# Kernel optimization log

Measured on AMD Instinct MI355X. Metric: run time of the kernel, lower is better.

The kernel has to match this reference:

```python
import jax, jax.numpy as jnp
import numpy as np

B, S, D_IN, D_MODEL = 128, 2048, 512, 2048
M, NSY, H, T = 25, 64, 8, 10
REP = NSY * (NSY + 1) // 2
OUT_DIMS = S * 2
DH = D_IN // H
IU, JU = np.triu_indices(NSY)
IDX_OUT = np.arange(NSY)                      # 'first-last': first n neurons for out sync
IDX_ACT = np.arange(D_MODEL - NSY, D_MODEL)   # last n neurons for action sync


def _ln(x, g, b):
    mu = x.mean(-1, keepdims=True)
    var = x.var(-1, keepdims=True)
    return (x - mu) / jnp.sqrt(var + 1e-5) * g + b


def _sync(act, alpha, beta, r, idx):
    # pairwise upper-triangle outer product without materializing (B,n,n)
    sel = act[:, idx]
    pair = sel[:, IU] * sel[:, JU]  # (B, REP)
    if alpha is None:
        alpha, beta = pair, jnp.ones_like(pair)
    else:
        alpha = r * alpha + pair
        beta = r * beta + 1.0
    return alpha / jnp.sqrt(beta), alpha, beta


def _forward(tokens, emb, W_pos, b_pos, Wq, bq, Wk, bk, Wv, bv, Wo, bo, Ws, bs,
             ln_s_g, ln_s_b, ln_n_g, ln_n_b, Wn, bn, temp, Wout, bout,
             start_act, start_trace, decay_action, decay_out):
    # rotary-style learned positional embedding: rotate [0,1] by theta in [0,180deg]
    thetas = jnp.deg2rad(jnp.linspace(0.0, 180.0, S))
    rotated = jnp.stack([-jnp.sin(thetas), jnp.cos(thetas)], -1)  # (S,2)
    pe = rotated @ W_pos + b_pos                                   # (S, D_IN)
    feats = emb[tokens] + pe[None]                                 # (B,S,D_IN)
    kh = (feats @ Wk + bk).reshape(B, S, H, DH)
    vh = (feats @ Wv + bv).reshape(B, S, H, DH)
    r_a = jnp.exp(-decay_action)[None]
    r_o = jnp.exp(-decay_out)[None]
    act = jnp.broadcast_to(start_act[None], (B, D_MODEL))
    trace = jnp.broadcast_to(start_trace[None], (B, D_MODEL, M))
    a_a = b_a = a_o = b_o = None
    preds, certs = [], []
    for _ in range(T):
        s_act, a_a, b_a = _sync(act, a_a, b_a, r_a, IDX_ACT)
        q = (s_act @ Wq + bq).reshape(B, H, DH)
        scores = jnp.einsum('bhd,bshd->bhs', q, kh) / np.float32(np.sqrt(DH))
        attn = jax.nn.softmax(scores, -1)
        o = jnp.einsum('bhs,bshd->bhd', attn, vh).reshape(B, D_IN) @ Wo + bo
        # SynapseNet: Linear -> GLU -> LayerNorm
        pre = jnp.concatenate([o, act], -1) @ Ws + bs
        g1, g2 = jnp.split(pre, 2, -1)
        state = _ln(g1 * jax.nn.sigmoid(g2), ln_s_g, ln_s_b)  # (B, D_MODEL)
        trace = jnp.concatenate([trace[:, :, 1:], state[:, :, None]], -1)
        # NLM: per-neuron linear over memory, GLU, temperature
        xn = _ln(trace, ln_n_g, ln_n_b)
        y = jnp.einsum('bnm,mon->bno', xn, Wn) + bn  # (B, D_MODEL, 2)
        act = (y[..., 0] * jax.nn.sigmoid(y[..., 1])) / temp
        s_out, a_o, b_o = _sync(act, a_o, b_o, r_o, IDX_OUT)
        pred = s_out @ Wout + bout  # (B, OUT_DIMS)
        preds.append(pred)
        logits = pred.reshape(B, S, 2)
        p = jax.nn.softmax(logits, -1)
        ent = -(p * jax.nn.log_softmax(logits, -1)).sum(-1) / np.float32(np.log(2.0))
        ne = ent.mean(-1)
        certs.append(jnp.stack([ne, 1.0 - ne], -1))
    return jnp.stack(preds, -1), jnp.stack(certs, -1)  # (B,OUT_DIMS,T),(B,2,T)


def setup_inputs() -> dict:
    key = jax.random.key(0)
    ks = jax.random.split(key, 16)
    def n(k, shape, s=0.02):
        return (jax.random.normal(k, shape) * s).astype(jnp.float32)
    bound = 1.0 / np.sqrt(M + 2)
    return {
        'tokens': jax.random.randint(ks[0], (B, S), 0, 2, dtype=jnp.int32),
        'emb': n(ks[1], (2, D_IN), 1.0),
        'W_pos': n(ks[2], (2, D_IN)), 'b_pos': jnp.zeros((D_IN,)),
        'Wq': n(ks[3], (REP, D_IN)), 'bq': jnp.zeros((D_IN,)),
        'Wk': n(ks[4], (D_IN, D_IN)), 'bk': jnp.zeros((D_IN,)),
        'Wv': n(ks[5], (D_IN, D_IN)), 'bv': jnp.zeros((D_IN,)),
        'Wo': n(ks[6], (D_IN, D_IN)), 'bo': jnp.zeros((D_IN,)),
        'Ws': n(ks[7], (D_IN + D_MODEL, 2 * D_MODEL)), 'bs': jnp.zeros((2 * D_MODEL,)),
        'ln_s_g': jnp.ones((D_MODEL,)), 'ln_s_b': jnp.zeros((D_MODEL,)),
        'ln_n_g': jnp.ones((M,)), 'ln_n_b': jnp.zeros((M,)),
        'Wn': jax.random.uniform(ks[8], (M, 2, D_MODEL), minval=-bound, maxval=bound),
        'bn': jnp.zeros((1, D_MODEL, 2)),
        'temp': jnp.ones((1,)),
        'Wout': n(ks[9], (REP, OUT_DIMS)), 'bout': jnp.zeros((OUT_DIMS,)),
        'start_act': n(ks[10], (D_MODEL,), 1.0),
        'start_trace': n(ks[11], (D_MODEL, M), 1.0),
        'decay_action': jax.random.uniform(ks[12], (REP,), minval=0.0, maxval=1.0),
        'decay_out': jax.random.uniform(ks[13], (REP,), minval=0.0, maxval=1.0),
    }


def reference(tokens, emb, W_pos, b_pos, Wq, bq, Wk, bk, Wv, bv, Wo, bo, Ws, bs,
              ln_s_g, ln_s_b, ln_n_g, ln_n_b, Wn, bn, temp, Wout, bout,
              start_act, start_trace, decay_action, decay_out):
    return _forward(tokens, emb, W_pos, b_pos, Wq, bq, Wk, bk, Wv, bv, Wo, bo, Ws, bs,
                    ln_s_g, ln_s_b, ln_n_g, ln_n_b, Wn, bn, temp, Wout, bout,
                    start_act, start_trace, decay_action, decay_out)
```

## Files before the change

kernel.cpp:

```cpp
#include <hip/hip_runtime.h>
#include <hip/hip_bf16.h>
#include <math.h>

#define B_ 128
#define S_ 2048
#define D_IN_ 512
#define D_MODEL_ 2048
#define M_ 25
#define NSY_ 64
#define H_ 8
#define T_ 10
#define REP_ 2080
#define DH_ 64
#define PRED_N (B_ * 4096)

typedef unsigned short ushort_t;
typedef __bf16 bf16x8 __attribute__((ext_vector_type(8)));
typedef float f32x4 __attribute__((ext_vector_type(4)));
typedef unsigned short us8 __attribute__((ext_vector_type(8)));
typedef unsigned short us4 __attribute__((ext_vector_type(4)));

__device__ __forceinline__ ushort_t f2bf(float f) {
    __hip_bfloat16 h = __float2bfloat16(f);
    return *(ushort_t*)&h;
}

__global__ __launch_bounds__(256) void gemm_bf16(
    const float* __restrict__ A, int lda,
    const ushort_t* __restrict__ Bt, int ldb,
    const float* __restrict__ bias,
    float* __restrict__ C, int ldc,
    int M, int N, int K, int kchunk)
{
    const int nb = blockIdx.x, mb = blockIdx.y, zb = blockIdx.z;
    const int k0 = zb * kchunk;
    const int k1 = min(K, k0 + kchunk);
    __shared__ ushort_t As[64][40];
    __shared__ ushort_t Bs[128][40];

    const int tid  = threadIdx.x;
    const int wave = tid >> 6;
    const int lane = tid & 63;
    const int quad = lane >> 4;
    const int mrow = lane & 15;

    f32x4 acc[4][2];
    #pragma unroll
    for (int s = 0; s < 4; s++)
        #pragma unroll
        for (int u = 0; u < 2; u++)
            acc[s][u] = (f32x4){0.f, 0.f, 0.f, 0.f};

    const int arow = tid >> 2, akc = (tid & 3) * 8;
    const int brow = tid >> 1, bkc = (tid & 1) * 16;

    for (int kk0 = k0; kk0 < k1; kk0 += 32) {
        {
            const float* ap = A + (size_t)(mb * 64 + arow) * lda + kk0 + akc;
            float4 v0 = *(const float4*)ap;
            float4 v1 = *(const float4*)(ap + 4);
            us8 w = { f2bf(v0.x), f2bf(v0.y), f2bf(v0.z), f2bf(v0.w),
                      f2bf(v1.x), f2bf(v1.y), f2bf(v1.z), f2bf(v1.w) };
            *(us8*)&As[arow][akc] = w;
        }
        {
            const ushort_t* bp = Bt + (size_t)(nb * 128 + brow) * ldb + kk0 + bkc;
            *(us8*)&Bs[brow][bkc]     = *(const us8*)bp;
            *(us8*)&Bs[brow][bkc + 8] = *(const us8*)(bp + 8);
        }
        __syncthreads();

        bf16x8 af[4], bfr[2];
        #pragma unroll
        for (int s = 0; s < 4; s++)
            af[s] = *(const bf16x8*)&As[s * 16 + mrow][quad * 8];
        #pragma unroll
        for (int u = 0; u < 2; u++)
            bfr[u] = *(const bf16x8*)&Bs[wave * 32 + u * 16 + mrow][quad * 8];
        #pragma unroll
        for (int s = 0; s < 4; s++)
            #pragma unroll
            for (int u = 0; u < 2; u++)
                acc[s][u] = __builtin_amdgcn_mfma_f32_16x16x32_bf16(
                    af[s], bfr[u], acc[s][u], 0, 0, 0);
        __syncthreads();
    }

    if (gridDim.z == 1) {
        #pragma unroll
        for (int s = 0; s < 4; s++)
            #pragma unroll
            for (int u = 0; u < 2; u++) {
                const int col = nb * 128 + wave * 32 + u * 16 + mrow;
                #pragma unroll
                for (int reg = 0; reg < 4; reg++) {
                    const int row = mb * 64 + s * 16 + quad * 4 + reg;
                    C[(size_t)row * ldc + col] = acc[s][u][reg] + bias[col];
                }
            }
    } else {
        #pragma unroll
        for (int s = 0; s < 4; s++)
            #pragma unroll
            for (int u = 0; u < 2; u++) {
                const int col = nb * 128 + wave * 32 + u * 16 + mrow;
                #pragma unroll
                for (int reg = 0; reg < 4; reg++) {
                    const int row = mb * 64 + s * 16 + quad * 4 + reg;
                    atomicAdd(&C[(size_t)row * ldc + col], acc[s][u][reg]);
                }
            }
    }
}

__global__ __launch_bounds__(256) void gemm3_kernel(
    const float* __restrict__ f2,
    const ushort_t* __restrict__ WkT, const float* __restrict__ bk, float* __restrict__ Ktab,
    const ushort_t* __restrict__ WvT, const float* __restrict__ bv, float* __restrict__ Vtab,
    const ushort_t* __restrict__ WsT, const ushort_t* __restrict__ WoC,
    const float* __restrict__ zerov, float* __restrict__ Wcomb32)
{
    const int nb = blockIdx.x, mb = blockIdx.y, zs = blockIdx.z;
    const ushort_t* Bt = (zs == 0) ? WkT : (zs == 1) ? WvT : WoC;
    const float* bias  = (zs == 0) ? bk  : (zs == 1) ? bv  : zerov;
    float* C           = (zs == 0) ? Ktab : (zs == 1) ? Vtab : Wcomb32;

    __shared__ ushort_t As[64][40];
    __shared__ ushort_t Bs[128][40];

    const int tid  = threadIdx.x;
    const int wave = tid >> 6;
    const int lane = tid & 63;
    const int quad = lane >> 4;
    const int mrow = lane & 15;

    f32x4 acc[4][2];
    #pragma unroll
    for (int s = 0; s < 4; s++)
        #pragma unroll
        for (int u = 0; u < 2; u++)
            acc[s][u] = (f32x4){0.f, 0.f, 0.f, 0.f};

    const int arow = tid >> 2, akc = (tid & 3) * 8;
    const int brow = tid >> 1, bkc = (tid & 1) * 16;

    for (int kk0 = 0; kk0 < 512; kk0 += 32) {
        if (zs < 2) {
            const float* ap = f2 + (size_t)(mb * 64 + arow) * 512 + kk0 + akc;
            float4 v0 = *(const float4*)ap;
            float4 v1 = *(const float4*)(ap + 4);
            us8 w = { f2bf(v0.x), f2bf(v0.y), f2bf(v0.z), f2bf(v0.w),
                      f2bf(v1.x), f2bf(v1.y), f2bf(v1.z), f2bf(v1.w) };
            *(us8*)&As[arow][akc] = w;
        } else {
            const ushort_t* ap = WsT + (size_t)(mb * 64 + arow) * 2560 + kk0 + akc;
            *(us8*)&As[arow][akc] = *(const us8*)ap;
        }
        {
            const ushort_t* bp = Bt + (size_t)(nb * 128 + brow) * 512 + kk0 + bkc;
            *(us8*)&Bs[brow][bkc]     = *(const us8*)bp;
            *(us8*)&Bs[brow][bkc + 8] = *(const us8*)(bp + 8);
        }
        __syncthreads();

        bf16x8 af[4], bfr[2];
        #pragma unroll
        for (int s = 0; s < 4; s++)
            af[s] = *(const bf16x8*)&As[s * 16 + mrow][quad * 8];
        #pragma unroll
        for (int u = 0; u < 2; u++)
            bfr[u] = *(const bf16x8*)&Bs[wave * 32 + u * 16 + mrow][quad * 8];
        #pragma unroll
        for (int s = 0; s < 4; s++)
            #pragma unroll
            for (int u = 0; u < 2; u++)
                acc[s][u] = __builtin_amdgcn_mfma_f32_16x16x32_bf16(
                    af[s], bfr[u], acc[s][u], 0, 0, 0);
        __syncthreads();
    }

    #pragma unroll
    for (int s = 0; s < 4; s++)
        #pragma unroll
        for (int u = 0; u < 2; u++) {
            const int col = nb * 128 + wave * 32 + u * 16 + mrow;
            #pragma unroll
            for (int reg = 0; reg < 4; reg++) {
                const int row = mb * 64 + s * 16 + quad * 4 + reg;
                C[(size_t)row * 512 + col] = acc[s][u][reg] + bias[col];
            }
        }
}

__device__ __forceinline__ void g_tile128(
    const ushort_t* Ap, int lda, const ushort_t* Bt, int ldb,
    float* C, int ldc, int nb, int mb, int k0, int k1, char* smem, int tid)
{
    ushort_t (*As)[40] = (ushort_t(*)[40])smem;
    ushort_t (*Bs)[40] = (ushort_t(*)[40])(smem + 64 * 40 * 2);
    const int wave = tid >> 6;
    const int lane = tid & 63;
    const int quad = lane >> 4;
    const int mrow = lane & 15;

    f32x4 acc[4][2];
    #pragma unroll
    for (int s = 0; s < 4; s++)
        #pragma unroll
        for (int u = 0; u < 2; u++)
            acc[s][u] = (f32x4){0.f, 0.f, 0.f, 0.f};

    const int arow = tid >> 2, akc = (tid & 3) * 8;
    const int brow = tid >> 1, bkc = (tid & 1) * 16;

    for (int kk0 = k0; kk0 < k1; kk0 += 32) {
        {
            const ushort_t* ap = Ap + (size_t)(mb * 64 + arow) * lda + kk0 + akc;
            *(us8*)&As[arow][akc] = *(const us8*)ap;
        }
        {
            const ushort_t* bp = Bt + (size_t)(nb * 128 + brow) * ldb + kk0 + bkc;
            *(us8*)&Bs[brow][bkc]     = *(const us8*)bp;
            *(us8*)&Bs[brow][bkc + 8] = *(const us8*)(bp + 8);
        }
        __syncthreads();

        bf16x8 af[4], bfr[2];
        #pragma unroll
        for (int s = 0; s < 4; s++)
            af[s] = *(const bf16x8*)&As[s * 16 + mrow][quad * 8];
        #pragma unroll
        for (int u = 0; u < 2; u++)
            bfr[u] = *(const bf16x8*)&Bs[wave * 32 + u * 16 + mrow][quad * 8];
        #pragma unroll
        for (int s = 0; s < 4; s++)
            #pragma unroll
            for (int u = 0; u < 2; u++)
                acc[s][u] = __builtin_amdgcn_mfma_f32_16x16x32_bf16(
                    af[s], bfr[u], acc[s][u], 0, 0, 0);
        __syncthreads();
    }

    #pragma unroll
    for (int s = 0; s < 4; s++)
        #pragma unroll
        for (int u = 0; u < 2; u++) {
            const int col = nb * 128 + wave * 32 + u * 16 + mrow;
            #pragma unroll
            for (int reg = 0; reg < 4; reg++) {
                const int row = mb * 64 + s * 16 + quad * 4 + reg;
                atomicAdd(&C[(size_t)row * ldc + col], acc[s][u][reg]);
            }
        }
}

__global__ __launch_bounds__(256) void triple_kernel(
    const ushort_t* __restrict__ s_outb, const ushort_t* __restrict__ WoutT,
    float* __restrict__ predt,
    const ushort_t* __restrict__ s_actb, const ushort_t* __restrict__ WqT,
    float* __restrict__ qbuf,
    const ushort_t* __restrict__ actb, const ushort_t* __restrict__ WsT,
    float* __restrict__ pre_nxt)
{
    __shared__ __align__(16) char smem[15360];
    const int vb = blockIdx.x, tid = threadIdx.x;
    if (vb < 320) {
        const int nb = vb & 31, mb = (vb >> 5) & 1, zb = vb >> 6;
        const int k0 = zb * 416;
        g_tile128(s_outb, REP_, WoutT, REP_, predt, 4096,
                  nb, mb, k0, min(REP_, k0 + 416), smem, tid);
    } else if (vb < 424) {
        const int v2 = vb - 320;
        const int nb = v2 & 3, mb = (v2 >> 2) & 1, zb = v2 >> 3;
        const int k0 = zb * 160;
        g_tile128(s_actb, REP_, WqT, REP_, qbuf, 512,
                  nb, mb, k0, min(REP_, k0 + 160), smem, tid);
    } else {
        const int v3 = vb - 424;
        const int nb = v3 & 31, mb = (v3 >> 5) & 1, zb = v3 >> 6;
        const int k0 = zb * 256;
        g_tile128(actb, 2048, WsT + 512, 2560, pre_nxt, 4096,
                  nb, mb, k0, k0 + 256, smem, tid);
    }
}

__global__ __launch_bounds__(256) void dual0_kernel(
    const ushort_t* __restrict__ actb, const ushort_t* __restrict__ WsT,
    float* __restrict__ pre0,
    const ushort_t* __restrict__ s_actb, const ushort_t* __restrict__ WqT,
    float* __restrict__ qbuf)
{
    __shared__ __align__(16) char smem[15360];
    const int vb = blockIdx.x, tid = threadIdx.x;
    if (vb < 512) {
        const int nb = vb & 31, mb = (vb >> 5) & 1, zb = vb >> 6;
        const int k0 = zb * 256;
        g_tile128(actb, 2048, WsT + 512, 2560, pre0, 4096,
                  nb, mb, k0, k0 + 256, smem, tid);
    } else {
        const int v2 = vb - 512;
        const int nb = v2 & 3, mb = (v2 >> 2) & 1, zb = v2 >> 3;
        const int k0 = zb * 160;
        g_tile128(s_actb, REP_, WqT, REP_, qbuf, 512,
                  nb, mb, k0, min(REP_, k0 + 160), smem, tid);
    }
}

__global__ __launch_bounds__(256) void gemm_qk_sel(
    const float* __restrict__ q,
    const ushort_t* __restrict__ Kb,
    const unsigned* __restrict__ tokbit,
    float* __restrict__ scsel)
{
    const int nb = blockIdx.x, mb = blockIdx.y, z = blockIdx.z;
    const int c = z >> 3, h = z & 7;
    __shared__ ushort_t As[64][40];
    __shared__ ushort_t Bs[128][40];

    const int tid  = threadIdx.x;
    const int wave = tid >> 6;
    const int lane = tid & 63;
    const int quad = lane >> 4;
    const int mrow = lane & 15;

    f32x4 acc[4][2];
    #pragma unroll
    for (int s = 0; s < 4; s++)
        #pragma unroll
        for (int u = 0; u < 2; u++)
            acc[s][u] = (f32x4){0.f, 0.f, 0.f, 0.f};

    const int arow = tid >> 2, akc = (tid & 3) * 8;
    const int brow = tid >> 1, bkc = (tid & 1) * 16;
    const float* Abase = q + (size_t)h * 64;
    const ushort_t* Bbase = Kb + (size_t)c * S_ * 512 + h * 64;

    #pragma unroll
    for (int kk0 = 0; kk0 < 64; kk0 += 32) {
        {
            const float* ap = Abase + (size_t)(mb * 64 + arow) * 512 + kk0 + akc;
            float4 v0 = *(const float4*)ap;
            float4 v1 = *(const float4*)(ap + 4);
            us8 w = { f2bf(v0.x), f2bf(v0.y), f2bf(v0.z), f2bf(v0.w),
                      f2bf(v1.x), f2bf(v1.y), f2bf(v1.z), f2bf(v1.w) };
            *(us8*)&As[arow][akc] = w;
        }
        {
            const ushort_t* bp = Bbase + (size_t)(nb * 128 + brow) * 512 + kk0 + bkc;
            *(us8*)&Bs[brow][bkc]     = *(const us8*)bp;
            *(us8*)&Bs[brow][bkc + 8] = *(const us8*)(bp + 8);
        }
        __syncthreads();

        bf16x8 af[4], bfr[2];
        #pragma unroll
        for (int s = 0; s < 4; s++)
            af[s] = *(const bf16x8*)&As[s * 16 + mrow][quad * 8];
        #pragma unroll
        for (int u = 0; u < 2; u++)
            bfr[u] = *(const bf16x8*)&Bs[wave * 32 + u * 16 + mrow][quad * 8];
        #pragma unroll
        for (int s = 0; s < 4; s++)
            #pragma unroll
            for (int u = 0; u < 2; u++)
                acc[s][u] = __builtin_amdgcn_mfma_f32_16x16x32_bf16(
                    af[s], bfr[u], acc[s][u], 0, 0, 0);
        __syncthreads();
    }

    const int colw = nb * 4 + wave;
    unsigned tb[16];
    #pragma unroll
    for (int s = 0; s < 4; s++)
        #pragma unroll
        for (int reg = 0; reg < 4; reg++) {
            const int row = mb * 64 + s * 16 + quad * 4 + reg;
            tb[s * 4 + reg] = tokbit[row * 64 + colw];
        }

    float* Cb = scsel + (size_t)h * 128 * S_;
    #pragma unroll
    for (int s = 0; s < 4; s++)
        #pragma unroll
        for (int u = 0; u < 2; u++) {
            const int col = nb * 128 + wave * 32 + u * 16 + mrow;
            const int sh = (u * 16 + mrow) & 31;
            #pragma unroll
            for (int reg = 0; reg < 4; reg++) {
                const int row = mb * 64 + s * 16 + quad * 4 + reg;
                if (((tb[s * 4 + reg] >> sh) & 1u) == (unsigned)c)
                    Cb[(size_t)row * S_ + col] = 0.125f * acc[s][u][reg];
            }
        }
}

__global__ __launch_bounds__(256) void attn_soft(
    const float* __restrict__ scsel,
    const int*   __restrict__ tokens,
    ushort_t* __restrict__ P,
    float* __restrict__ o,
    const float* __restrict__ bs2,
    float* __restrict__ pre_nxt)
{
    const int bh = blockIdx.x;
    const int b = bh >> 3, h = bh & 7;
    __shared__ float red[256];
    const int tid = threadIdx.x;

    if (bh < 512) {
        const int idx = bh * 256 + tid;
        const float4* bs4 = (const float4*)bs2;
        ((float4*)pre_nxt)[idx] = bs4[idx & 1023];
    } else if (bh < 576) {
        const int idx = (bh - 512) * 256 + tid;
        ((float4*)o)[idx] = make_float4(0.f, 0.f, 0.f, 0.f);
    }

    const float* scs = scsel + ((size_t)h * 128 + b) * S_;
    const int* trow = tokens + (size_t)b * S_;

    int tok[8]; float sel[8];
    float lmax = -1e30f;
    #pragma unroll
    for (int i = 0; i < 8; i++) {
        const int s = tid + i * 256;
        tok[i] = trow[s];
        sel[i] = scs[s];
        lmax = fmaxf(lmax, sel[i]);
    }
    red[tid] = lmax; __syncthreads();
    for (int off = 128; off > 0; off >>= 1) {
        if (tid < off) red[tid] = fmaxf(red[tid], red[tid + off]);
        __syncthreads();
    }
    const float mx = red[0];
    __syncthreads();

    float e[8];
    float lsum = 0.f;
    #pragma unroll
    for (int i = 0; i < 8; i++) {
        e[i] = expf(sel[i] - mx);
        lsum += e[i];
    }
    red[tid] = lsum; __syncthreads();
    for (int off = 128; off > 0; off >>= 1) {
        if (tid < off) red[tid] += red[tid + off];
        __syncthreads();
    }
    const float inv = 1.f / red[0];

    ushort_t* Pb = P + ((size_t)h * 128 + b) * 4096;
    #pragma unroll
    for (int i = 0; i < 8; i++) {
        const int s = tid + i * 256;
        const unsigned p = (unsigned)f2bf(e[i] * inv);
        const unsigned word = tok[i] ? (p << 16) : p;
        *(unsigned*)&Pb[s * 2] = word;
    }
}

__global__ __launch_bounds__(256) void gemm_pv(
    const ushort_t* __restrict__ P,
    const ushort_t* __restrict__ VT,
    float* __restrict__ o)
{
    const int mb = blockIdx.x, h = blockIdx.y, zb = blockIdx.z;
    const int k0 = zb * 256;
    __shared__ ushort_t As[64][40];
    __shared__ ushort_t Bs[64][40];

    const int tid  = threadIdx.x;
    const int wave = tid >> 6;
    const int lane = tid & 63;
    const int quad = lane >> 4;
    const int mrow = lane & 15;

    f32x4 acc[4];
    #pragma unroll
    for (int s = 0; s < 4; s++) acc[s] = (f32x4){0.f, 0.f, 0.f, 0.f};

    const int row = tid >> 2, kc = (tid & 3) * 8;
    const ushort_t* Ab = P  + ((size_t)h * 128 + mb * 64 + row) * 4096;
    const ushort_t* Bb = VT + ((size_t)h * 64 + row) * 4096;

    for (int kk = k0; kk < k0 + 256; kk += 32) {
        *(us8*)&As[row][kc] = *(const us8*)(Ab + kk + kc);
        *(us8*)&Bs[row][kc] = *(const us8*)(Bb + kk + kc);
        __syncthreads();
        bf16x8 bfr = *(const bf16x8*)&Bs[wave * 16 + mrow][quad * 8];
        #pragma unroll
        for (int s = 0; s < 4; s++) {
            bf16x8 af = *(const bf16x8*)&As[s * 16 + mrow][quad * 8];
            acc[s] = __builtin_amdgcn_mfma_f32_16x16x32_bf16(af, bfr, acc[s], 0, 0, 0);
        }
        __syncthreads();
    }

    const int col = h * 64 + wave * 16 + mrow;
    #pragma unroll
    for (int s = 0; s < 4; s++)
        #pragma unroll
        for (int reg = 0; reg < 4; reg++) {
            const int rowi = mb * 64 + s * 16 + quad * 4 + reg;
            atomicAdd(&o[(size_t)rowi * 512 + col], acc[s][reg]);
        }
}

#define IA_FE 8192
#define IA_AC (IA_FE + 1024)
#define IA_TR (IA_AC + 6400)
#define IA_SY (IA_TR + 9)
#define IA_ZV (IA_SY + 1)
#define IA_WO (IA_ZV + 256)
#define IA_BS (IA_WO + 16)
#define IA_NB (IA_BS + 1024)
__global__ void init_all(const float* __restrict__ emb, const float* __restrict__ Wp,
                         const float* __restrict__ bp, float* __restrict__ f2,
                         const float* __restrict__ sa, float* __restrict__ act,
                         ushort_t* __restrict__ actb,
                         const float* __restrict__ st, float* __restrict__ trace,
                         const float* __restrict__ dec_act, const float* __restrict__ dec_out,
                         int* __restrict__ ijtab, float* __restrict__ r_act,
                         float* __restrict__ r_out, float* __restrict__ sqb_a,
                         float* __restrict__ sqb_o, float* __restrict__ zerov,
                         const float* __restrict__ Wo, ushort_t* __restrict__ WoC,
                         const float* __restrict__ bs, const float* __restrict__ bo,
                         const float* __restrict__ Ws, float* __restrict__ bs2,
                         const int* __restrict__ tokens, unsigned* __restrict__ tokbit)
{
    const int vb = blockIdx.x, tid = threadIdx.x;
    if (vb < IA_FE) {
        const int gid = vb * 256 + tid;
        const int k = gid & 511;
        const int s = (gid >> 9) & (S_ - 1);
        const int c = gid >> 20;
        const float th = 3.14159265358979323846f * (float)s / (float)(S_ - 1);
        f2[gid] = emb[c * 512 + k] + (-sinf(th)) * Wp[k] + cosf(th) * Wp[512 + k] + bp[k];
    } else if (vb < IA_AC) {
        const int gid = (vb - IA_FE) * 256 + tid;
        const int n = gid & 2047;
        const float v = sa[n];
        act[gid] = v;
        actb[gid] = f2bf(v);
    } else if (vb < IA_TR) {
        const int idx4 = (vb - IA_AC) * 256 + tid;
        ((float4*)trace)[idx4] = ((const float4*)st)[idx4 % 12800];
    } else if (vb < IA_SY) {
        const int p = (vb - IA_TR) * 256 + tid;
        if (p >= REP_) return;
        int i = 0, rem = p;
        while (rem >= NSY_ - i) { rem -= NSY_ - i; i++; }
        ijtab[p] = (i << 16) | (i + rem);
        const float ra = expf(-dec_act[p]);
        const float ro = expf(-dec_out[p]);
        r_act[p] = ra; r_out[p] = ro;
        float ba = 1.f, bo2 = 1.f;
        sqb_a[p] = 1.f;
        sqb_o[p] = 1.f;
        for (int t = 1; t < T_; t++) {
            ba  = ra * ba  + 1.f;
            bo2 = ro * bo2 + 1.f;
            sqb_a[(size_t)t * REP_ + p] = sqrtf(ba);
            sqb_o[(size_t)t * REP_ + p] = sqrtf(bo2);
        }
    } else if (vb < IA_ZV) {
        #pragma unroll
        for (int k = 0; k < 4; k++)
            ((float4*)zerov)[tid * 4 + k] = make_float4(0.f, 0.f, 0.f, 0.f);
    } else if (vb < IA_WO) {
        const int idx4 = (vb - IA_ZV) * 256 + tid;
        float4 v = ((const float4*)Wo)[idx4];
        us4 w = { f2bf(v.x), f2bf(v.y), f2bf(v.z), f2bf(v.w) };
        ((us4*)WoC)[idx4] = w;
    } else if (vb < IA_BS) {
        const int n = (vb - IA_WO) * 256 + tid;
        float acc = bs[n];
        for (int j = 0; j < 512; j++)
            acc += bo[j] * Ws[(size_t)j * 4096 + n];
        bs2[n] = acc;
    } else {
        const int blk = vb - IA_BS;
        const int b = blk >> 3, s0 = (blk & 7) * 256;
        const int tok = tokens[(size_t)b * S_ + s0 + tid];
        const unsigned long long m = __ballot(tok != 0);
        if ((tid & 63) == 0) {
            const int w = tid >> 6;
            tokbit[b * 64 + (s0 >> 5) + w * 2]     = (unsigned)m;
            tokbit[b * 64 + (s0 >> 5) + w * 2 + 1] = (unsigned)(m >> 32);
        }
    }
}

__global__ __launch_bounds__(256) void transpose_all(
    const float* __restrict__ Wk, ushort_t* __restrict__ WkT,
    const float* __restrict__ Wv, ushort_t* __restrict__ WvT,
    const float* __restrict__ Wq, ushort_t* __restrict__ WqT,
    const float* __restrict__ Wo, ushort_t* __restrict__ WoT,
    const float* __restrict__ Ws, ushort_t* __restrict__ WsT,
    const float* __restrict__ Wout, ushort_t* __restrict__ WoutT)
{
    int bid = blockIdx.x;
    const float* in; ushort_t* out; int K, N;
    if      (bid <   256) {              in = Wk;   out = WkT;   K = 512;  N = 512;  }
    else if (bid <   512) { bid -=  256; in = Wv;   out = WvT;   K = 512;  N = 512;  }
    else if (bid <  1552) { bid -=  512; in = Wq;   out = WqT;   K = 2080; N = 512;  }
    else if (bid <  1808) { bid -= 1552; in = Wo;   out = WoT;   K = 512;  N = 512;  }
    else if (bid < 12048) { bid -= 1808; in = Ws;   out = WsT;   K = 2560; N = 4096; }
    else                  { bid -= 12048; in = Wout; out = WoutT; K = 2080; N = 4096; }
    const int bxw = N >> 5;
    const int bx = bid % bxw, by = bid / bxw;
    __shared__ float tile[32][33];
    const int k0 = by * 32, n0 = bx * 32;
    const int tx = threadIdx.x & 31, ty4 = (threadIdx.x >> 5) * 4;
    #pragma unroll
    for (int i = 0; i < 4; i++)
        tile[ty4 + i][tx] = in[(size_t)(k0 + ty4 + i) * N + n0 + tx];
    __syncthreads();
    #pragma unroll
    for (int i = 0; i < 4; i++)
        out[(size_t)(n0 + ty4 + i) * K + k0 + tx] = f2bf(tile[tx][ty4 + i]);
}

__global__ void cast3_kernel(const float* __restrict__ Ktab, ushort_t* __restrict__ Kb,
                             const float* __restrict__ Vtab, ushort_t* __restrict__ VT,
                             const float* __restrict__ Wcomb32, ushort_t* __restrict__ WcombTb)
{
    const int vb = blockIdx.x, tid = threadIdx.x;
    if (vb < 2048) {
        const int idx4 = vb * 256 + tid;
        float4 v = ((const float4*)Ktab)[idx4];
        us4 w = { f2bf(v.x), f2bf(v.y), f2bf(v.z), f2bf(v.w) };
        ((us4*)Kb)[idx4] = w;
    } else if (vb < 10240) {
        const int gid = (vb - 2048) * 256 + tid;
        const int k = gid & 4095;
        const int d = (gid >> 12) & 63;
        const int h = gid >> 18;
        const int s = k >> 1, c = k & 1;
        VT[gid] = f2bf(Vtab[((size_t)(c * S_ + s)) * 512 + h * 64 + d]);
    } else {
        const int idx4 = (vb - 10240) * 256 + tid;
        float4 v = ((const float4*)Wcomb32)[idx4];
        us4 w = { f2bf(v.x), f2bf(v.y), f2bf(v.z), f2bf(v.w) };
        ((us4*)WcombTb)[idx4] = w;
    }
}

__global__ void sync_kernel(const float* __restrict__ act,
                            float* __restrict__ alpha,
                            const float* __restrict__ decay,
                            const int t, const int off,
                            ushort_t* __restrict__ sout,
                            float* __restrict__ ib1, const float* __restrict__ bias1, int iN1,
                            float* __restrict__ ib2, const float* __restrict__ bias2, int iN2)
{
    const int b = blockIdx.x;
    const int tid = threadIdx.x;
    if (blockIdx.y == 8) {
        if (ib1)
            for (int n = tid; n < iN1; n += 256)
                ib1[(size_t)b * iN1 + n] = bias1[n];
        if (ib2)
            for (int n = tid; n < iN2; n += 256)
                ib2[(size_t)b * iN2 + n] = bias2[n];
    }
    const int p = blockIdx.y * 256 + tid;
    if (p >= REP_) return;
    int i = 0, rem = p;
    while (rem >= NSY_ - i) { rem -= NSY_ - i; i++; }
    const int j = i + rem;
    const float si = act[(size_t)b * D_MODEL_ + off + i];
    const float sj = act[(size_t)b * D_MODEL_ + off + j];
    const float pair = si * sj;
    const float r = expf(-decay[p]);
    float a;
    if (t == 0) a = pair;
    else        a = r * alpha[(size_t)b * REP_ + p] + pair;
    alpha[(size_t)b * REP_ + p] = a;
    float bta = 1.f;
    for (int k = 0; k < t; k++) bta = r * bta + 1.f;
    sout[(size_t)b * REP_ + p] = f2bf(a / sqrtf(bta));
}

template<int TT>
__global__ __launch_bounds__(512, 2) void st_kernel(
    const float* __restrict__ pre,
    const float* __restrict__ g,
    const float* __restrict__ bt,
    float* __restrict__ trace,
    const float* __restrict__ ln_g,
    const float* __restrict__ ln_b,
    const float* __restrict__ Wn,
    const float* __restrict__ bn,
    const float* __restrict__ temp,
    ushort_t* __restrict__ actb,
    const int* __restrict__ ijtab,
    const float* __restrict__ r_out,
    const float* __restrict__ sqb_out,
    float* __restrict__ a_o,
    ushort_t* __restrict__ s_outb,
    const float* __restrict__ bout,
    float* __restrict__ predt,
    const float* __restrict__ r_act,
    const float* __restrict__ sqb_act,
    float* __restrict__ a_a,
    ushort_t* __restrict__ s_actb,
    const float* __restrict__ bq,
    float* __restrict__ qbuf)
{
    const int b = blockIdx.x >> 1, half = blockIdx.x & 1;
    const int tid = threadIdx.x;
    __shared__ float v[D_MODEL_];
    __shared__ float r1[512], r2[512];
    __shared__ float sh_sync[64];
    float s1 = 0.f, s2 = 0.f;
    #pragma unroll
    for (int i = 0; i < 4; i++) {
        const int dd = tid + i * 512;
        const float g1 = pre[(size_t)b * 4096 + dd];
        const float g2 = pre[(size_t)b * 4096 + 2048 + dd];
        const float val = g1 * (1.f / (1.f + expf(-g2)));
        v[dd] = val; s1 += val; s2 += val * val;
    }
    r1[tid] = s1; r2[tid] = s2; __syncthreads();
    for (int off = 256; off > 0; off >>= 1) {
        if (tid < off) { r1[tid] += r1[tid + off]; r2[tid] += r2[tid + off]; }
        __syncthreads();
    }
    const float mu = r1[0] * (1.f / D_MODEL_);
    const float var = fmaxf(r2[0] * (1.f / D_MODEL_) - mu * mu, 0.f);
    const float sinv = 1.f / sqrtf(var + 1e-5f);
    const float tval = temp[0];

    #pragma unroll
    for (int i = 0; i < 2; i++) {
        const int n = half * 1024 + i * 512 + tid;
        const float sval = (v[n] - mu) * sinv * g[n] + bt[n];
        const int gid = b * 2048 + n;
        float* tr = trace + (size_t)gid * M_;
        float x[M_];
        #pragma unroll
        for (int m = 0; m < M_ - 1; m++) {
            int slot = TT + 1 + m;
            if (slot >= M_) slot -= M_;
            x[m] = tr[slot];
        }
        x[M_ - 1] = sval;
        tr[TT] = sval;
        float t1 = 0.f, t2 = 0.f;
        #pragma unroll
        for (int m = 0; m < M_; m++) { t1 += x[m]; t2 += x[m] * x[m]; }
        const float tmu = t1 * (1.f / M_);
        const float tvar = fmaxf(t2 * (1.f / M_) - tmu * tmu, 0.f);
        const float tinv = 1.f / sqrtf(tvar + 1e-5f);
        float y0 = bn[n * 2 + 0], y1 = bn[n * 2 + 1];
        #pragma unroll
        for (int m = 0; m < M_; m++) {
            const float xn = (x[m] - tmu) * tinv * ln_g[m] + ln_b[m];
            y0 += xn * Wn[(size_t)(m * 2 + 0) * D_MODEL_ + n];
            y1 += xn * Wn[(size_t)(m * 2 + 1) * D_MODEL_ + n];
        }
        const float a = y0 * (1.f / (1.f + expf(-y1))) / tval;
        actb[gid] = f2bf(a);
        if (half == 0) {
            if (i == 0 && tid < 64) sh_sync[tid] = a;
        } else {
            if (i == 1 && tid >= 448) sh_sync[tid - 448] = a;
        }
    }
    __syncthreads();

    if (half == 0) {
        for (int p = tid; p < REP_; p += 512) {
            const int ij = ijtab[p];
            const float pair = sh_sync[ij >> 16] * sh_sync[ij & 0xffff];
            const float r = r_out[p];
            float a2;
            if (TT == 0) a2 = pair;
            else         a2 = r * a_o[(size_t)b * REP_ + p] + pair;
            a_o[(size_t)b * REP_ + p] = a2;
            s_outb[(size_t)b * REP_ + p] = f2bf(a2 / sqb_out[(size_t)TT * REP_ + p]);
        }
        const float4* b4 = (const float4*)bout;
        float4* pd = (float4*)(predt + (size_t)b * 4096);
        for (int idx = tid; idx < 1024; idx += 512) pd[idx] = b4[idx];
    } else if (TT < T_ - 1) {
        for (int p = tid; p < REP_; p += 512) {
            const int ij = ijtab[p];
            const float pair = sh_sync[ij >> 16] * sh_sync[ij & 0xffff];
            const float r = r_act[p];
            float a2 = r * a_a[(size_t)b * REP_ + p] + pair;
            a_a[(size_t)b * REP_ + p] = a2;
            s_actb[(size_t)b * REP_ + p] = f2bf(a2 / sqb_act[(size_t)(TT + 1) * REP_ + p]);
        }
        const float4* b4 = (const float4*)bq;
        float4* qb = (float4*)(qbuf + (size_t)b * 512);
        if (tid < 128) qb[tid] = b4[tid];
    }
}

__global__ __launch_bounds__(256) void epilogue_kernel(
    const float* __restrict__ predst,
    float* __restrict__ dout)
{
    __shared__ float tile[T_][1024];
    __shared__ float red[256];
    __shared__ float certv[T_];
    const int b = blockIdx.x, tid = threadIdx.x;

    float esum[T_];
    #pragma unroll
    for (int t = 0; t < T_; t++) esum[t] = 0.f;

    for (int c4 = 0; c4 < 4; c4++) {
        const int row0 = c4 * 1024;
        #pragma unroll
        for (int t = 0; t < T_; t++) {
            float4 v = *(const float4*)(predst + (size_t)t * PRED_N
                                        + (size_t)b * 4096 + row0 + tid * 4);
            tile[t][tid * 4 + 0] = v.x; tile[t][tid * 4 + 1] = v.y;
            tile[t][tid * 4 + 2] = v.z; tile[t][tid * 4 + 3] = v.w;
            {
                const float mm = fmaxf(v.x, v.y);
                const float z0 = expf(v.x - mm), z1 = expf(v.y - mm);
                const float Z = z0 + z1, lz = logf(Z);
                const float p0 = z0 / Z, p1 = z1 / Z;
                esum[t] += -(p0 * ((v.x - mm) - lz) + p1 * ((v.y - mm) - lz))
                           * 1.4426950408889634f;
            }
            {
                const float mm = fmaxf(v.z, v.w);
                const float z0 = expf(v.z - mm), z1 = expf(v.w - mm);
                const float Z = z0 + z1, lz = logf(Z);
                const float p0 = z0 / Z, p1 = z1 / Z;
                esum[t] += -(p0 * ((v.z - mm) - lz) + p1 * ((v.w - mm) - lz))
                           * 1.4426950408889634f;
            }
        }
        __syncthreads();
        float buf[40];
        #pragma unroll
        for (int r = 0; r < 4; r++)
            #pragma unroll
            for (int t = 0; t < T_; t++)
                buf[r * 10 + t] = tile[t][tid * 4 + r];
        float* dst = dout + ((size_t)b * 4096 + row0 + tid * 4) * T_;
        #pragma unroll
        for (int k = 0; k < 10; k++)
            *(float4*)(dst + k * 4) = make_float4(buf[4*k], buf[4*k+1], buf[4*k+2], buf[4*k+3]);
        __syncthreads();
    }

    #pragma unroll
    for (int t = 0; t < T_; t++) {
        red[tid] = esum[t]; __syncthreads();
        for (int off = 128; off > 0; off >>= 1) {
            if (tid < off) red[tid] += red[tid + off];
            __syncthreads();
        }
        if (tid == 0) certv[t] = red[0] * (1.f / S_);
        __syncthreads();
    }

    const size_t base = (size_t)PRED_N * T_;
    if (tid < T_)
        dout[base + (size_t)(b * 2 + 0) * T_ + tid] = certv[tid];
    else if (tid < 2 * T_)
        dout[base + (size_t)(b * 2 + 1) * T_ + (tid - T_)] = 1.f - certv[tid - T_];
}

extern "C" void kernel_launch(void* const* d_in, const int* in_sizes, int n_in,
                              void* d_out, int out_size, void* d_ws, size_t ws_size,
                              hipStream_t stream)
{
    const int*   tokens    = (const int*)  d_in[0];
    const float* emb       = (const float*)d_in[1];
    const float* W_pos     = (const float*)d_in[2];
    const float* b_pos     = (const float*)d_in[3];
    const float* Wq        = (const float*)d_in[4];
    const float* bq        = (const float*)d_in[5];
    const float* Wk        = (const float*)d_in[6];
    const float* bk        = (const float*)d_in[7];
    const float* Wv        = (const float*)d_in[8];
    const float* bv        = (const float*)d_in[9];
    const float* Wo        = (const float*)d_in[10];
    const float* bo        = (const float*)d_in[11];
    const float* Ws        = (const float*)d_in[12];
    const float* bs        = (const float*)d_in[13];
    const float* ln_s_g    = (const float*)d_in[14];
    const float* ln_s_b    = (const float*)d_in[15];
    const float* ln_n_g    = (const float*)d_in[16];
    const float* ln_n_b    = (const float*)d_in[17];
    const float* Wn        = (const float*)d_in[18];
    const float* bn        = (const float*)d_in[19];
    const float* temp      = (const float*)d_in[20];
    const float* Wout      = (const float*)d_in[21];
    const float* bout      = (const float*)d_in[22];
    const float* start_act = (const float*)d_in[23];
    const float* start_tr  = (const float*)d_in[24];
    const float* dec_act   = (const float*)d_in[25];
    const float* dec_out   = (const float*)d_in[26];
    float* out = (float*)d_out;
    float* w = (float*)d_ws;

    size_t off = 0;
    float* f2     = w + off; off += (size_t)2 * S_ * 512;
    float* Ktab   = w + off; off += (size_t)2 * S_ * 512;
    float* Vtab   = w + off; off += (size_t)2 * S_ * 512;
    float* act    = w + off; off += (size_t)B_ * D_MODEL_;
    float* a_a    = w + off; off += (size_t)B_ * REP_;
    float* a_o    = w + off; off += (size_t)B_ * REP_;
    float* qbuf   = w + off; off += (size_t)B_ * 512;
    float* o_attn = w + off; off += (size_t)B_ * 512;
    float* pre0   = w + off; off += (size_t)B_ * 4096;
    float* pre1   = w + off; off += (size_t)B_ * 4096;
    float* trace  = w + off; off += (size_t)B_ * D_MODEL_ * M_;
    float* scsel  = w + off; off += (size_t)8 * 128 * S_;
    float* predst = w + off; off += (size_t)T_ * PRED_N;
    float* Wcomb32= w + off; off += (size_t)4096 * 512;
    float* bs2    = w + off; off += 4096;
    float* zerov  = w + off; off += 4096;
    ushort_t* s_actb = (ushort_t*)(w + off); off += (size_t)B_ * REP_ / 2;
    ushort_t* s_outb = (ushort_t*)(w + off); off += (size_t)B_ * REP_ / 2;
    ushort_t* actb   = (ushort_t*)(w + off); off += (size_t)B_ * D_MODEL_ / 2;
    __hip_bfloat16* Kb = (__hip_bfloat16*)(w + off); off += (size_t)S_ * 512;
    ushort_t* Pbuf  = (ushort_t*)(w + off); off += (size_t)8 * 128 * 4096 / 2;
    ushort_t* VT    = (ushort_t*)(w + off); off += (size_t)8 * 64 * 4096 / 2;
    ushort_t* WkT   = (ushort_t*)(w + off); off += (size_t)512 * 512 / 2;
    ushort_t* WvT   = (ushort_t*)(w + off); off += (size_t)512 * 512 / 2;
    ushort_t* WqT   = (ushort_t*)(w + off); off += (size_t)512 * REP_ / 2;
    ushort_t* WoT   = (ushort_t*)(w + off); off += (size_t)512 * 512 / 2;
    ushort_t* WsT   = (ushort_t*)(w + off); off += (size_t)4096 * 2560 / 2;
    ushort_t* WoutT = (ushort_t*)(w + off); off += (size_t)4096 * REP_ / 2;
    ushort_t* WoC   = (ushort_t*)(w + off); off += (size_t)512 * 512 / 2;
    ushort_t* WcombTb=(ushort_t*)(w + off); off += (size_t)4096 * 512 / 2;
    int*   ijtab  = (int*)(w + off); off += REP_;
    float* r_actT = w + off; off += REP_;
    float* r_outT = w + off; off += REP_;
    float* sqb_a  = w + off; off += (size_t)T_ * REP_;
    float* sqb_o  = w + off; off += (size_t)T_ * REP_;
    unsigned* tokbit = (unsigned*)(w + off); off += (size_t)B_ * 64 / 1;

    init_all<<<IA_NB, 256, 0, stream>>>(
        emb, W_pos, b_pos, f2, start_act, act, actb, start_tr, trace,
        dec_act, dec_out, ijtab, r_actT, r_outT, sqb_a, sqb_o, zerov,
        Wo, WoC, bs, bo, Ws, bs2, tokens, tokbit);
    transpose_all<<<20368, 256, 0, stream>>>(
        Wk, WkT, Wv, WvT, Wq, WqT, Wo, WoT, Ws, WsT, Wout, WoutT);
    gemm3_kernel<<<dim3(4, 64, 3), 256, 0, stream>>>(
        f2, WkT, bk, Ktab, WvT, bv, Vtab, WsT, WoC, zerov, Wcomb32);
    cast3_kernel<<<12288, 256, 0, stream>>>(
        Ktab, (ushort_t*)Kb, Vtab, VT, Wcomb32, WcombTb);
    sync_kernel<<<dim3(B_, 9), 256, 0, stream>>>(
        act, a_a, dec_act, 0, D_MODEL_ - NSY_, s_actb,
        qbuf, bq, 512, pre0, bs2, 4096);
    dual0_kernel<<<616, 256, 0, stream>>>(actb, WsT, pre0, s_actb, WqT, qbuf);

    #define ST_ARGS(PC, PT) \
        PC, ln_s_g, ln_s_b, trace, ln_n_g, ln_n_b, Wn, bn, temp, actb, \
        ijtab, r_outT, sqb_o, a_o, s_outb, bout, PT, \
        r_actT, sqb_a, a_a, s_actb, bq, qbuf

    for (int t = 0; t < T_; t++) {
        float* pre_cur = (t & 1) ? pre1 : pre0;
        float* pre_nxt = (t & 1) ? pre0 : pre1;
        float* predt = predst + (size_t)t * PRED_N;

        gemm_qk_sel<<<dim3(S_ / 128, 2, 16), 256, 0, stream>>>(
            qbuf, (const ushort_t*)Kb, tokbit, scsel);
        attn_soft<<<B_ * H_, 256, 0, stream>>>(
            scsel, tokens, Pbuf, o_attn, bs2, pre_nxt);
        gemm_pv<<<dim3(2, 8, 16), 256, 0, stream>>>(Pbuf, VT, o_attn);

        gemm_bf16<<<dim3(32, 2, 4), 256, 0, stream>>>(
            o_attn, 512, WcombTb, 512, bs2, pre_cur, 4096, B_, 4096, 512, 128);

        switch (t) {
            case 0: st_kernel<0><<<B_ * 2, 512, 0, stream>>>(ST_ARGS(pre_cur, predt)); break;
            case 1: st_kernel<1><<<B_ * 2, 512, 0, stream>>>(ST_ARGS(pre_cur, predt)); break;
            case 2: st_kernel<2><<<B_ * 2, 512, 0, stream>>>(ST_ARGS(pre_cur, predt)); break;
            case 3: st_kernel<3><<<B_ * 2, 512, 0, stream>>>(ST_ARGS(pre_cur, predt)); break;
            case 4: st_kernel<4><<<B_ * 2, 512, 0, stream>>>(ST_ARGS(pre_cur, predt)); break;
            case 5: st_kernel<5><<<B_ * 2, 512, 0, stream>>>(ST_ARGS(pre_cur, predt)); break;
            case 6: st_kernel<6><<<B_ * 2, 512, 0, stream>>>(ST_ARGS(pre_cur, predt)); break;
            case 7: st_kernel<7><<<B_ * 2, 512, 0, stream>>>(ST_ARGS(pre_cur, predt)); break;
            case 8: st_kernel<8><<<B_ * 2, 512, 0, stream>>>(ST_ARGS(pre_cur, predt)); break;
            case 9: st_kernel<9><<<B_ * 2, 512, 0, stream>>>(ST_ARGS(pre_cur, predt)); break;
        }

        const int nblk = (t < T_ - 1) ? 936 : 320;
        triple_kernel<<<nblk, 256, 0, stream>>>(
            s_outb, WoutT, predt, s_actb, WqT, qbuf, actb, WsT, pre_nxt);
    }

    epilogue_kernel<<<B_, 256, 0, stream>>>(predst, out);
}
```

Baseline: 1.113 ms.

## Fuse both token-class QK passes into one kernel and parallelize epilogue

The QK score kernel now computes scores against both K tables (token bit 0 and 1) in a single block, sharing the Q tile, and selects per element from the token bitmask. This halves the grid and removes the predicated store pattern. The softmax kernel reads the packed token bitmask instead of full int tokens. The epilogue is split over 4x more blocks, with certainty sums accumulated atomically and finalized by a small extra kernel. The trade-offs are higher register and LDS use in the QK kernel, plus one extra launch and atomics.

```diff
diff --git a/kernel.cpp b/kernel.cpp
--- a/kernel.cpp
+++ b/kernel.cpp
@@ -306,16 +306,16 @@
     }
 }
 
-__global__ __launch_bounds__(256) void gemm_qk_sel(
+__global__ __launch_bounds__(256) void gemm_qk2(
     const float* __restrict__ q,
     const ushort_t* __restrict__ Kb,
     const unsigned* __restrict__ tokbit,
     float* __restrict__ scsel)
 {
-    const int nb = blockIdx.x, mb = blockIdx.y, z = blockIdx.z;
-    const int c = z >> 3, h = z & 7;
+    const int nb = blockIdx.x, mb = blockIdx.y, h = blockIdx.z;
     __shared__ ushort_t As[64][40];
-    __shared__ ushort_t Bs[128][40];
+    __shared__ ushort_t Bs0[128][40];
+    __shared__ ushort_t Bs1[128][40];
 
     const int tid  = threadIdx.x;
     const int wave = tid >> 6;
@@ -323,17 +323,20 @@
     const int quad = lane >> 4;
     const int mrow = lane & 15;
 
-    f32x4 acc[4][2];
+    f32x4 acc0[4][2], acc1[4][2];
     #pragma unroll
     for (int s = 0; s < 4; s++)
         #pragma unroll
-        for (int u = 0; u < 2; u++)
-            acc[s][u] = (f32x4){0.f, 0.f, 0.f, 0.f};
+        for (int u = 0; u < 2; u++) {
+            acc0[s][u] = (f32x4){0.f, 0.f, 0.f, 0.f};
+            acc1[s][u] = (f32x4){0.f, 0.f, 0.f, 0.f};
+        }
 
     const int arow = tid >> 2, akc = (tid & 3) * 8;
     const int brow = tid >> 1, bkc = (tid & 1) * 16;
     const float* Abase = q + (size_t)h * 64;
-    const ushort_t* Bbase = Kb + (size_t)c * S_ * 512 + h * 64;
+    const ushort_t* Bbase0 = Kb + (size_t)h * 64;
+    const ushort_t* Bbase1 = Kb + (size_t)S_ * 512 + h * 64;
 
     #pragma unroll
     for (int kk0 = 0; kk0 < 64; kk0 += 32) {
@@ -346,25 +349,34 @@
             *(us8*)&As[arow][akc] = w;
         }
         {
-            const ushort_t* bp = Bbase + (size_t)(nb * 128 + brow) * 512 + kk0 + bkc;
-            *(us8*)&Bs[brow][bkc]     = *(const us8*)bp;
-            *(us8*)&Bs[brow][bkc + 8] = *(const us8*)(bp + 8);
-        }
-        __syncthreads();
-
-        bf16x8 af[4], bfr[2];
+            const size_t boff = (size_t)(nb * 128 + brow) * 512 + kk0 + bkc;
+            const ushort_t* bp0 = Bbase0 + boff;
+            const ushort_t* bp1 = Bbase1 + boff;
+            *(us8*)&Bs0[brow][bkc]     = *(const us8*)bp0;
+            *(us8*)&Bs0[brow][bkc + 8] = *(const us8*)(bp0 + 8);
+            *(us8*)&Bs1[brow][bkc]     = *(const us8*)bp1;
+            *(us8*)&Bs1[brow][bkc + 8] = *(const us8*)(bp1 + 8);
+        }
+        __syncthreads();
+
+        bf16x8 af[4], bf0[2], bf1[2];
         #pragma unroll
         for (int s = 0; s < 4; s++)
             af[s] = *(const bf16x8*)&As[s * 16 + mrow][quad * 8];
         #pragma unroll
-        for (int u = 0; u < 2; u++)
-            bfr[u] = *(const bf16x8*)&Bs[wave * 32 + u * 16 + mrow][quad * 8];
+        for (int u = 0; u < 2; u++) {
+            bf0[u] = *(const bf16x8*)&Bs0[wave * 32 + u * 16 + mrow][quad * 8];
+            bf1[u] = *(const bf16x8*)&Bs1[wave * 32 + u * 16 + mrow][quad * 8];
+        }
         #pragma unroll
         for (int s = 0; s < 4; s++)
             #pragma unroll
-            for (int u = 0; u < 2; u++)
-                acc[s][u] = __builtin_amdgcn_mfma_f32_16x16x32_bf16(
-                    af[s], bfr[u], acc[s][u], 0, 0, 0);
+            for (int u = 0; u < 2; u++) {
+                acc0[s][u] = __builtin_amdgcn_mfma_f32_16x16x32_bf16(
+                    af[s], bf0[u], acc0[s][u], 0, 0, 0);
+                acc1[s][u] = __builtin_amdgcn_mfma_f32_16x16x32_bf16(
+                    af[s], bf1[u], acc1[s][u], 0, 0, 0);
+            }
         __syncthreads();
     }
 
@@ -384,19 +396,20 @@
         #pragma unroll
         for (int u = 0; u < 2; u++) {
             const int col = nb * 128 + wave * 32 + u * 16 + mrow;
-            const int sh = (u * 16 + mrow) & 31;
+            const int sh = u * 16 + mrow;
             #pragma unroll
             for (int reg = 0; reg < 4; reg++) {
                 const int row = mb * 64 + s * 16 + quad * 4 + reg;
-                if (((tb[s * 4 + reg] >> sh) & 1u) == (unsigned)c)
-                    Cb[(size_t)row * S_ + col] = 0.125f * acc[s][u][reg];
+                const bool one = (tb[s * 4 + reg] >> sh) & 1u;
+                const float val = one ? acc1[s][u][reg] : acc0[s][u][reg];
+                Cb[(size_t)row * S_ + col] = 0.125f * val;
             }
         }
 }
 
 __global__ __launch_bounds__(256) void attn_soft(
     const float* __restrict__ scsel,
-    const int*   __restrict__ tokens,
+    const unsigned* __restrict__ tokbit,
     ushort_t* __restrict__ P,
     float* __restrict__ o,
     const float* __restrict__ bs2,
@@ -417,14 +430,14 @@
     }
 
     const float* scs = scsel + ((size_t)h * 128 + b) * S_;
-    const int* trow = tokens + (size_t)b * S_;
-
-    int tok[8]; float sel[8];
+    const unsigned* tw = tokbit + b * 64;
+
+    unsigned tok[8]; float sel[8];
     float lmax = -1e30f;
     #pragma unroll
     for (int i = 0; i < 8; i++) {
         const int s = tid + i * 256;
-        tok[i] = trow[s];
+        tok[i] = (tw[s >> 5] >> (s & 31)) & 1u;
         sel[i] = scs[s];
         lmax = fmaxf(lmax, sel[i]);
     }
@@ -514,7 +527,8 @@
 #define IA_ZV (IA_SY + 1)
 #define IA_WO (IA_ZV + 256)
 #define IA_BS (IA_WO + 16)
-#define IA_NB (IA_BS + 1024)
+#define IA_TB (IA_BS + 1024)
+#define IA_NB (IA_TB + 1)
 __global__ void init_all(const float* __restrict__ emb, const float* __restrict__ Wp,
                          const float* __restrict__ bp, float* __restrict__ f2,
                          const float* __restrict__ sa, float* __restrict__ act,
@@ -527,7 +541,8 @@
                          const float* __restrict__ Wo, ushort_t* __restrict__ WoC,
                          const float* __restrict__ bs, const float* __restrict__ bo,
                          const float* __restrict__ Ws, float* __restrict__ bs2,
-                         const int* __restrict__ tokens, unsigned* __restrict__ tokbit)
+                         const int* __restrict__ tokens, unsigned* __restrict__ tokbit,
+                         float* __restrict__ certacc)
 {
     const int vb = blockIdx.x, tid = threadIdx.x;
     if (vb < IA_FE) {
@@ -579,7 +594,7 @@
         for (int j = 0; j < 512; j++)
             acc += bo[j] * Ws[(size_t)j * 4096 + n];
         bs2[n] = acc;
-    } else {
+    } else if (vb < IA_TB) {
         const int blk = vb - IA_BS;
         const int b = blk >> 3, s0 = (blk & 7) * 256;
         const int tok = tokens[(size_t)b * S_ + s0 + tid];
@@ -588,6 +603,12 @@
             const int w = tid >> 6;
             tokbit[b * 64 + (s0 >> 5) + w * 2]     = (unsigned)m;
             tokbit[b * 64 + (s0 >> 5) + w * 2 + 1] = (unsigned)(m >> 32);
+        }
+    } else {
+        #pragma unroll
+        for (int k = 0; k < 5; k++) {
+            const int id = tid + k * 256;
+            if (id < B_ * T_) certacc[id] = 0.f;
         }
     }
 }
@@ -802,55 +823,55 @@
 
 __global__ __launch_bounds__(256) void epilogue_kernel(
     const float* __restrict__ predst,
-    float* __restrict__ dout)
+    float* __restrict__ dout,
+    float* __restrict__ certacc)
 {
     __shared__ float tile[T_][1024];
     __shared__ float red[256];
-    __shared__ float certv[T_];
-    const int b = blockIdx.x, tid = threadIdx.x;
+    const int blk = blockIdx.x;
+    const int b = blk >> 2, c4 = blk & 3;
+    const int tid = threadIdx.x;
+    const int row0 = c4 * 1024;
 
     float esum[T_];
     #pragma unroll
-    for (int t = 0; t < T_; t++) esum[t] = 0.f;
-
-    for (int c4 = 0; c4 < 4; c4++) {
-        const int row0 = c4 * 1024;
-        #pragma unroll
-        for (int t = 0; t < T_; t++) {
-            float4 v = *(const float4*)(predst + (size_t)t * PRED_N
-                                        + (size_t)b * 4096 + row0 + tid * 4);
-            tile[t][tid * 4 + 0] = v.x; tile[t][tid * 4 + 1] = v.y;
-            tile[t][tid * 4 + 2] = v.z; tile[t][tid * 4 + 3] = v.w;
-            {
-                const float mm = fmaxf(v.x, v.y);
-                const float z0 = expf(v.x - mm), z1 = expf(v.y - mm);
-                const float Z = z0 + z1, lz = logf(Z);
-                const float p0 = z0 / Z, p1 = z1 / Z;
-                esum[t] += -(p0 * ((v.x - mm) - lz) + p1 * ((v.y - mm) - lz))
-                           * 1.4426950408889634f;
-            }
-            {
-                const float mm = fmaxf(v.z, v.w);
-                const float z0 = expf(v.z - mm), z1 = expf(v.w - mm);
-                const float Z = z0 + z1, lz = logf(Z);
-                const float p0 = z0 / Z, p1 = z1 / Z;
-                esum[t] += -(p0 * ((v.z - mm) - lz) + p1 * ((v.w - mm) - lz))
-                           * 1.4426950408889634f;
-            }
-        }
-        __syncthreads();
-        float buf[40];
-        #pragma unroll
-        for (int r = 0; r < 4; r++)
-            #pragma unroll
-            for (int t = 0; t < T_; t++)
-                buf[r * 10 + t] = tile[t][tid * 4 + r];
-        float* dst = dout + ((size_t)b * 4096 + row0 + tid * 4) * T_;
-        #pragma unroll
-        for (int k = 0; k < 10; k++)
-            *(float4*)(dst + k * 4) = make_float4(buf[4*k], buf[4*k+1], buf[4*k+2], buf[4*k+3]);
-        __syncthreads();
-    }
+    for (int t = 0; t < T_; t++) {
+        float4 v = *(const float4*)(predst + (size_t)t * PRED_N
+                                    + (size_t)b * 4096 + row0 + tid * 4);
+        tile[t][tid * 4 + 0] = v.x; tile[t][tid * 4 + 1] = v.y;
+        tile[t][tid * 4 + 2] = v.z; tile[t][tid * 4 + 3] = v.w;
+        float es;
+        {
+            const float mm = fmaxf(v.x, v.y);
+            const float z0 = expf(v.x - mm), z1 = expf(v.y - mm);
+            const float Z = z0 + z1, lz = logf(Z);
+            const float p0 = z0 / Z, p1 = z1 / Z;
+            es = -(p0 * ((v.x - mm) - lz) + p1 * ((v.y - mm) - lz))
+                 * 1.4426950408889634f;
+        }
+        {
+            const float mm = fmaxf(v.z, v.w);
+            const float z0 = expf(v.z - mm), z1 = expf(v.w - mm);
+            const float Z = z0 + z1, lz = logf(Z);
+            const float p0 = z0 / Z, p1 = z1 / Z;
+            es += -(p0 * ((v.z - mm) - lz) + p1 * ((v.w - mm) - lz))
+                  * 1.4426950408889634f;
+        }
+        esum[t] = es;
+    }
+    __syncthreads();
+
+    float buf[40];
+    #pragma unroll
+    for (int r = 0; r < 4; r++)
+        #pragma unroll
+        for (int t = 0; t < T_; t++)
+            buf[r * 10 + t] = tile[t][tid * 4 + r];
+    float* dst = dout + ((size_t)b * 4096 + row0 + tid * 4) * T_;
+    #pragma unroll
+    for (int k = 0; k < 10; k++)
+        *(float4*)(dst + k * 4) = make_float4(buf[4*k], buf[4*k+1], buf[4*k+2], buf[4*k+3]);
+    __syncthreads();
 
     #pragma unroll
     for (int t = 0; t < T_; t++) {
@@ -859,15 +880,26 @@
             if (tid < off) red[tid] += red[tid + off];
             __syncthreads();
         }
-        if (tid == 0) certv[t] = red[0] * (1.f / S_);
-        __syncthreads();
-    }
-
+        if (tid == 0) atomicAdd(&certacc[b * T_ + t], red[0]);
+        __syncthreads();
+    }
+}
+
+__global__ void cert_kernel(const float* __restrict__ certacc,
+                            float* __restrict__ dout)
+{
+    const int tid = threadIdx.x;
     const size_t base = (size_t)PRED_N * T_;
-    if (tid < T_)
-        dout[base + (size_t)(b * 2 + 0) * T_ + tid] = certv[tid];
-    else if (tid < 2 * T_)
-        dout[base + (size_t)(b * 2 + 1) * T_ + (tid - T_)] = 1.f - certv[tid - T_];
+    #pragma unroll
+    for (int k = 0; k < 5; k++) {
+        const int id = tid + k * 256;
+        if (id < B_ * T_) {
+            const int b = id / T_, t = id % T_;
+            const float ne = certacc[id] * (1.f / S_);
+            dout[base + (size_t)(b * 2 + 0) * T_ + t] = ne;
+            dout[base + (size_t)(b * 2 + 1) * T_ + t] = 1.f - ne;
+        }
+    }
 }
 
 extern "C" void kernel_launch(void* const* d_in, const int* in_sizes, int n_in,
@@ -921,6 +953,7 @@
     float* Wcomb32= w + off; off += (size_t)4096 * 512;
     float* bs2    = w + off; off += 4096;
     float* zerov  = w + off; off += 4096;
+    float* certacc= w + off; off += (size_t)B_ * T_;
     ushort_t* s_actb = (ushort_t*)(w + off); off += (size_t)B_ * REP_ / 2;
     ushort_t* s_outb = (ushort_t*)(w + off); off += (size_t)B_ * REP_ / 2;
     ushort_t* actb   = (ushort_t*)(w + off); off += (size_t)B_ * D_MODEL_ / 2;
@@ -940,12 +973,12 @@
     float* r_outT = w + off; off += REP_;
     float* sqb_a  = w + off; off += (size_t)T_ * REP_;
     float* sqb_o  = w + off; off += (size_t)T_ * REP_;
-    unsigned* tokbit = (unsigned*)(w + off); off += (size_t)B_ * 64 / 1;
+    unsigned* tokbit = (unsigned*)(w + off); off += (size_t)B_ * 64;
 
     init_all<<<IA_NB, 256, 0, stream>>>(
         emb, W_pos, b_pos, f2, start_act, act, actb, start_tr, trace,
         dec_act, dec_out, ijtab, r_actT, r_outT, sqb_a, sqb_o, zerov,
-        Wo, WoC, bs, bo, Ws, bs2, tokens, tokbit);
+        Wo, WoC, bs, bo, Ws, bs2, tokens, tokbit, certacc);
     transpose_all<<<20368, 256, 0, stream>>>(
         Wk, WkT, Wv, WvT, Wq, WqT, Wo, WoT, Ws, WsT, Wout, WoutT);
     gemm3_kernel<<<dim3(4, 64, 3), 256, 0, stream>>>(
@@ -967,10 +1000,10 @@
         float* pre_nxt = (t & 1) ? pre0 : pre1;
         float* predt = predst + (size_t)t * PRED_N;
 
-        gemm_qk_sel<<<dim3(S_ / 128, 2, 16), 256, 0, stream>>>(
+        gemm_qk2<<<dim3(S_ / 128, 2, 8), 256, 0, stream>>>(
             qbuf, (const ushort_t*)Kb, tokbit, scsel);
         attn_soft<<<B_ * H_, 256, 0, stream>>>(
-            scsel, tokens, Pbuf, o_attn, bs2, pre_nxt);
+            scsel, tokbit, Pbuf, o_attn, bs2, pre_nxt);
         gemm_pv<<<dim3(2, 8, 16), 256, 0, stream>>>(Pbuf, VT, o_attn);
 
         gemm_bf16<<<dim3(32, 2, 4), 256, 0, stream>>>(
@@ -994,5 +1027,6 @@
             s_outb, WoutT, predt, s_actb, WqT, qbuf, actb, WsT, pre_nxt);
     }
 
-    epilogue_kernel<<<B_, 256, 0, stream>>>(predst, out);
-}
+    epilogue_kernel<<<512, 256, 0, stream>>>(predst, out, certacc);
+    cert_kernel<<<1, 256, 0, stream>>>(certacc, out);
+}
```

Measured after the change: 1.232 ms. +10.7%, slower.
